# Optimization experiments

Hardware: AMD Instinct MI355X
Metric: run time of the kernel (lower is better)

## Reference

```python
import jax, jax.numpy as jnp
import numpy as np

MODES = 32
INPUT_MODES = 24
LAMBDA = 0.1
T_TOTAL = 1.0
EVAL_PTS = 200  # hardcoded in Circuit.forward


def _unitary_from_parameters(n, params):
    # Reconstruct a unitary from n**2-1 real SU(N)-generator coefficients:
    # Hermitian traceless H, then U = expm(iH) via eigh (differentiable).
    m = n * (n - 1) // 2
    re = params[:m]
    im = params[m:2 * m]
    d = params[2 * m:2 * m + n - 1]
    iu = jnp.triu_indices(n, 1)
    H = jnp.zeros((n, n), jnp.complex64).at[iu].set(re + 1j * im)
    H = H + H.conj().T
    diag = jnp.concatenate([d, -jnp.sum(d, keepdims=True)]).astype(jnp.complex64)
    H = H + jnp.diag(diag)
    w, V = jnp.linalg.eigh(H)  # H Hermitian
    return (V * jnp.exp(1j * w)[None, :]) @ V.conj().T


def setup_inputs() -> dict:
    key = jax.random.key(0)
    k1, k2, k3, k4, k5, k6 = jax.random.split(key, 6)
    B = 2048
    return {
        "A0_real": jax.random.normal(k1, (B, INPUT_MODES), jnp.float32),
        "A0_imag": jax.random.normal(k2, (B, INPUT_MODES), jnp.float32),
        "omega": jax.random.normal(k3, (MODES,), jnp.float32),
        "kappa": jax.random.uniform(k4, (MODES,), jnp.float32),
        "nonlinearity": jax.random.uniform(k5, (1,), jnp.float32),
        "params": (jax.random.uniform(k6, (MODES * MODES - 1,), jnp.float32) - 0.5) * (2.0 * np.pi),
    }


def reference(A0_real, A0_imag, omega, kappa, nonlinearity, params):
    c64 = jnp.complex64
    B = A0_real.shape[0]
    A0 = (A0_real + 1j * A0_imag).astype(c64)
    # pad: first input_modes from A0, rest ones (per forward)
    A_init = jnp.ones((B, MODES), c64).at[:, :INPUT_MODES].set(A0)

    U = _unitary_from_parameters(MODES, params)
    I = jnp.eye(MODES, dtype=c64)
    UtU = U.T @ U  # plain (non-conjugate) transpose, matching torch U.T
    mix = UtU @ jnp.linalg.inv(I * (1.0 + LAMBDA) - UtU)
    kappa2 = kappa.astype(c64) ** 2            # ode passes kappa**2
    sk = jnp.sqrt(kappa2)                      # diag_embed(kappa**0.5)
    T2 = -(sk[:, None] * (0.5 * I + mix)) * sk[None, :]  # constant in time
    nl2 = (nonlinearity[0].astype(c64)) ** 2   # ode passes nonlinearity**2
    om = omega.astype(c64)

    def f(A):  # time_evolution_operator, with diag matmuls fused elementwise
        freq = 1j * (om[None, :] + nl2 * (jnp.abs(A) ** 2))  # [B, modes]
        return freq * A + A @ T2.T  # correct_norm assumed identity passthrough

    dt = T_TOTAL / (EVAL_PTS - 1)

    def step(A, _):  # classic RK4 (fixed-step stand-in for dopri5)
        k1 = f(A)
        k2 = f(A + 0.5 * dt * k1)
        k3 = f(A + 0.5 * dt * k2)
        k4 = f(A + dt * k3)
        A = A + (dt / 6.0) * (k1 + 2.0 * k2 + 2.0 * k3 + k4)
        return A, A

    _, traj = jax.lax.scan(step, A_init, None, length=EVAL_PTS - 1)
    return jnp.concatenate([A_init[None], traj], axis=0)  # [200, B, modes] complex64
```

## Files before the change

kernel.cpp:

```cpp
#include <hip/hip_runtime.h>
#include <math.h>

#define NMODES 32
#define NPAIR 496
#define TAYLOR_N 12

__device__ float2 g_T2[NMODES * NMODES];

__device__ __forceinline__ float2 cmul(float2 a, float2 b) {
    return make_float2(a.x * b.x - a.y * b.y, a.x * b.y + a.y * b.x);
}

__global__ __launch_bounds__(1024) void setup_kernel(const float* __restrict__ params,
                                                     const float* __restrict__ kappa) {
    __shared__ float2 X[NMODES][NMODES];
    __shared__ float2 R[NMODES][NMODES];
    __shared__ float2 W[NMODES][NMODES];
    __shared__ float2 Aug[NMODES][2 * NMODES];
    __shared__ int sh_s;
    __shared__ float sh_scale;
    __shared__ int sh_piv;
    __shared__ float2 sh_pivrec;

    const int tid = threadIdx.x;
    const int i = tid >> 5;
    const int j = tid & 31;

    float2 h;
    if (i == j) {
        float d;
        if (i < 31) {
            d = params[2 * NPAIR + i];
        } else {
            d = 0.0f;
            for (int r = 0; r < 31; ++r) d -= params[2 * NPAIR + r];
        }
        h = make_float2(d, 0.0f);
    } else {
        int a = (i < j) ? i : j;
        int b = (i < j) ? j : i;
        int idx = 31 * a - (a * (a - 1)) / 2 + (b - a - 1);
        float re = params[idx];
        float im = params[NPAIR + idx];
        h = (i < j) ? make_float2(re, im) : make_float2(re, -im);
    }
    X[i][j] = h;
    __syncthreads();

    if (tid < 32) {
        float s = 0.0f;
        for (int c = 0; c < NMODES; ++c) {
            float2 v = X[tid][c];
            s += sqrtf(v.x * v.x + v.y * v.y);
        }
        for (int off = 16; off > 0; off >>= 1)
            s = fmaxf(s, __shfl_down(s, off));
        if (tid == 0) {
            int sc_n = 0;
            float sc = 1.0f;
            while (s > 0.25f && sc_n < 40) { s *= 0.5f; sc *= 0.5f; ++sc_n; }
            sh_s = sc_n;
            sh_scale = sc;
        }
    }
    __syncthreads();

    {
        float sc = sh_scale;
        float2 v = X[i][j];
        X[i][j] = make_float2(-v.y * sc, v.x * sc);
    }
    __syncthreads();

    R[i][j] = make_float2((i == j) ? 1.0f : 0.0f, 0.0f);
    __syncthreads();
    for (int k = TAYLOR_N; k >= 1; --k) {
        float2 acc = make_float2(0.0f, 0.0f);
        for (int kk = 0; kk < NMODES; ++kk) {
            float2 a = X[i][kk];
            float2 b = R[kk][j];
            acc.x = fmaf(a.x, b.x, fmaf(-a.y, b.y, acc.x));
            acc.y = fmaf(a.x, b.y, fmaf(a.y, b.x, acc.y));
        }
        __syncthreads();
        float invk = 1.0f / (float)k;
        R[i][j] = make_float2(((i == j) ? 1.0f : 0.0f) + acc.x * invk, acc.y * invk);
        __syncthreads();
    }

    {
        int s = sh_s;
        for (int q = 0; q < s; ++q) {
            float2 acc = make_float2(0.0f, 0.0f);
            for (int kk = 0; kk < NMODES; ++kk) {
                float2 a = R[i][kk];
                float2 b = R[kk][j];
                acc.x = fmaf(a.x, b.x, fmaf(-a.y, b.y, acc.x));
                acc.y = fmaf(a.x, b.y, fmaf(a.y, b.x, acc.y));
            }
            __syncthreads();
            R[i][j] = acc;
            __syncthreads();
        }
    }

    {
        float2 acc = make_float2(0.0f, 0.0f);
        for (int kk = 0; kk < NMODES; ++kk) {
            float2 a = R[kk][i];
            float2 b = R[kk][j];
            acc.x = fmaf(a.x, b.x, fmaf(-a.y, b.y, acc.x));
            acc.y = fmaf(a.x, b.y, fmaf(a.y, b.x, acc.y));
        }
        W[i][j] = acc;
    }
    __syncthreads();

    {
        float2 w = W[i][j];
        Aug[i][j] = make_float2(((i == j) ? 1.1f : 0.0f) - w.x, -w.y);
        Aug[i][j + NMODES] = w;
    }
    __syncthreads();

    for (int p = 0; p < NMODES; ++p) {
        if (tid < 32) {
            float2 v = Aug[tid][p];
            float mag = (tid >= p) ? (v.x * v.x + v.y * v.y) : -1.0f;
            int idx = tid;
            for (int off = 16; off > 0; off >>= 1) {
                float omg = __shfl_down(mag, off);
                int oi = __shfl_down(idx, off);
                if (omg > mag) { mag = omg; idx = oi; }
            }
            if (tid == 0) sh_piv = idx;
        }
        __syncthreads();
        int piv = sh_piv;
        if (piv != p && i == p) {
            float2 a0 = Aug[p][j], b0 = Aug[piv][j];
            float2 a1 = Aug[p][j + NMODES], b1 = Aug[piv][j + NMODES];
            Aug[p][j] = b0; Aug[piv][j] = a0;
            Aug[p][j + NMODES] = b1; Aug[piv][j + NMODES] = a1;
        }
        __syncthreads();
        if (tid == 0) {
            float2 d = Aug[p][p];
            float den = d.x * d.x + d.y * d.y;
            sh_pivrec = make_float2(d.x / den, -d.y / den);
        }
        __syncthreads();
        if (i == p) {
            float2 pr = sh_pivrec;
            Aug[p][j] = cmul(Aug[p][j], pr);
            Aug[p][j + NMODES] = cmul(Aug[p][j + NMODES], pr);
        }
        __syncthreads();
        float2 f = Aug[i][p];
        __syncthreads();
        if (i != p) {
            float2 rp0 = Aug[p][j];
            float2 rp1 = Aug[p][j + NMODES];
            float2 v0 = Aug[i][j];
            float2 v1 = Aug[i][j + NMODES];
            v0.x -= f.x * rp0.x - f.y * rp0.y;
            v0.y -= f.x * rp0.y + f.y * rp0.x;
            v1.x -= f.x * rp1.x - f.y * rp1.y;
            v1.y -= f.x * rp1.y + f.y * rp1.x;
            Aug[i][j] = v0;
            Aug[i][j + NMODES] = v1;
        }
        __syncthreads();
    }

    {
        float2 mix = Aug[i][j + NMODES];
        float kk2 = fabsf(kappa[i]) * fabsf(kappa[j]);
        float re = -kk2 * (((i == j) ? 0.5f : 0.0f) + mix.x);
        float im = -kk2 * mix.y;
        g_T2[i * NMODES + j] = make_float2(re, im);
    }
}

template<int CTRL>
__device__ __forceinline__ float2 dppshuf(float2 v) {
    return make_float2(
        __int_as_float(__builtin_amdgcn_mov_dpp(__float_as_int(v.x), CTRL, 0xF, 0xF, true)),
        __int_as_float(__builtin_amdgcn_mov_dpp(__float_as_int(v.y), CTRL, 0xF, 0xF, true)));
}

#define QP_X1 0xB1
#define QP_X2 0x4E
#define QP_X3 0x1B
#define HM_X7 0x141
#define RM_XF 0x140

__device__ __forceinline__ void cfma(float2& acc, float2 c, float2 w) {
    acc.x = fmaf(c.x, w.x, fmaf(-c.y, w.y, acc.x));
    acc.y = fmaf(c.x, w.y, fmaf(c.y, w.x, acc.y));
}

__device__ __forceinline__ float bperm(int idx, float v) {
    return __int_as_float(__builtin_amdgcn_ds_bpermute(idx, __float_as_int(v)));
}

__device__ __forceinline__ float2 feval(const float2* __restrict__ t2,
                                        float2 z, float om, float nl2,
                                        int bp0, int bp1) {
    float2 w1 = dppshuf<QP_X1>(z);
    float2 w2 = dppshuf<QP_X2>(z);
    float2 w3 = dppshuf<QP_X3>(z);
    float2 w7 = dppshuf<HM_X7>(z);
    float2 wF = dppshuf<RM_XF>(z);
    float2 w4 = dppshuf<QP_X3>(w7);
    float2 w5 = dppshuf<QP_X2>(w7);
    float2 w6 = dppshuf<QP_X1>(w7);
    float2 w8 = dppshuf<HM_X7>(wF);
    float2 wC = dppshuf<QP_X3>(wF);
    float2 wD = dppshuf<QP_X2>(wF);
    float2 wE = dppshuf<QP_X1>(wF);
    float2 w9 = dppshuf<QP_X1>(w8);
    float2 wA = dppshuf<QP_X2>(w8);
    float2 wB = dppshuf<QP_X3>(w8);

    float2 a0 = make_float2(0.0f, 0.0f), a1 = make_float2(0.0f, 0.0f);
    float2 a2 = make_float2(0.0f, 0.0f), a3 = make_float2(0.0f, 0.0f);
    cfma(a0, t2[0],  z);
    cfma(a1, t2[1],  w1);
    cfma(a2, t2[2],  w2);
    cfma(a3, t2[3],  w3);
    cfma(a0, t2[4],  w4);
    cfma(a1, t2[5],  w5);
    cfma(a2, t2[6],  w6);
    cfma(a3, t2[7],  w7);
    cfma(a0, t2[8],  w8);
    cfma(a1, t2[9],  w9);
    cfma(a2, t2[10], wA);
    cfma(a3, t2[11], wB);
    cfma(a0, t2[12], wC);
    cfma(a1, t2[13], wD);
    cfma(a2, t2[14], wE);
    cfma(a3, t2[15], wF);

    float px = (a0.x + a1.x) + (a2.x + a3.x);
    float py = (a0.y + a1.y) + (a2.y + a3.y);
    float kx = bperm(bp0, px) + bperm(bp1, px);
    float ky = bperm(bp0, py) + bperm(bp1, py);

    float wf = fmaf(nl2, fmaf(z.x, z.x, z.y * z.y), om);
    return make_float2(kx - wf * z.y, ky + wf * z.x);
}

__global__ __launch_bounds__(64) void ode_kernel(const float* __restrict__ A0r,
                                                 const float* __restrict__ A0i,
                                                 const float* __restrict__ omega,
                                                 const float* __restrict__ nln,
                                                 float* __restrict__ out,
                                                 long long out_size) {
    const int lane = threadIdx.x;
    const int r = lane >> 4;
    const int p = lane & 15;
    const int ho = r & 1;
    const int hr = (r == 1 || r == 2) ? 1 : 0;
    const int mstar = 16 * hr + p;
    const int bp0 = 4 * mstar;
    const int bp1 = bp0 + 128;
    const int b = blockIdx.x;

    float2 t2[16];
    {
        const int row_g = 16 * ho + p;
#pragma unroll
        for (int s = 0; s < 16; ++s)
            t2[s] = g_T2[row_g * 32 + 16 * hr + (p ^ s)];
    }

    const float om = omega[mstar];
    const float nl = nln[0];
    const float nl2 = nl * nl;
    const float dt = 1.0f / 199.0f;
    const float hdt = 0.5f * dt;
    const float sdt = dt / 6.0f;

    __shared__ float2 ainit[32];
    if (lane < 32) {
        float2 v;
        if (lane < 24) v = make_float2(A0r[b * 24 + lane], A0i[b * 24 + lane]);
        else           v = make_float2(1.0f, 0.0f);
        ainit[lane] = v;
    }
    __syncthreads();
    float2 a = ainit[mstar];

    long long o = (long long)b * 32 + lane;
    if (lane < 32 && o < out_size) out[o] = a.x;

    for (int t = 1; t < 200; ++t) {
        float2 k1 = feval(t2, a, om, nl2, bp0, bp1);
        float2 z = make_float2(fmaf(hdt, k1.x, a.x), fmaf(hdt, k1.y, a.y));
        float2 k2 = feval(t2, z, om, nl2, bp0, bp1);
        z = make_float2(fmaf(hdt, k2.x, a.x), fmaf(hdt, k2.y, a.y));
        float2 k3 = feval(t2, z, om, nl2, bp0, bp1);
        z = make_float2(fmaf(dt, k3.x, a.x), fmaf(dt, k3.y, a.y));
        float2 k4 = feval(t2, z, om, nl2, bp0, bp1);

        a.x = fmaf(sdt, fmaf(2.0f, k2.x + k3.x, k1.x + k4.x), a.x);
        a.y = fmaf(sdt, fmaf(2.0f, k2.y + k3.y, k1.y + k4.y), a.y);

        o += 65536;
        if (lane < 32 && o < out_size) out[o] = a.x;
    }
}

extern "C" void kernel_launch(void* const* d_in, const int* in_sizes, int n_in,
                              void* d_out, int out_size, void* d_ws, size_t ws_size,
                              hipStream_t stream) {
    const float* A0r = (const float*)d_in[0];
    const float* A0i = (const float*)d_in[1];
    const float* omega = (const float*)d_in[2];
    const float* kappa = (const float*)d_in[3];
    const float* nln = (const float*)d_in[4];
    const float* params = (const float*)d_in[5];

    setup_kernel<<<1, 1024, 0, stream>>>(params, kappa);
    ode_kernel<<<2048, 64, 0, stream>>>(A0r, A0i, omega, nln,
                                        (float*)d_out, (long long)out_size);
}
```

Baseline: 395.3 us.

## Replace bpermute reductions with permlane32/16 swaps and remap lanes per mode

Remaps the 64 lanes so each half-wave owns all 32 modes, with the two halves holding complementary column halves of T2. The cross-half reduction now uses permlane32_swap instead of two ds_bpermute ops. The shuffle seed comes from a permlane16_swap (or ds_swizzle fallback) so the DPP butterfly covers the right column block. The aim is to take LDS-routed permutes off the serial RK4 dependency chain, at the cost of one extra cross-lane op per stage and reliance on gfx950-specific builtins.

```diff
diff --git a/kernel.cpp b/kernel.cpp
--- a/kernel.cpp
+++ b/kernel.cpp
@@ -195,6 +195,8 @@
 #define HM_X7 0x141
 #define RM_XF 0x140
 
+typedef unsigned int v2u __attribute__((ext_vector_type(2)));
+
 __device__ __forceinline__ void cfma(float2& acc, float2 c, float2 w) {
     acc.x = fmaf(c.x, w.x, fmaf(-c.y, w.y, acc.x));
     acc.y = fmaf(c.x, w.y, fmaf(c.y, w.x, acc.y));
@@ -204,14 +206,47 @@
     return __int_as_float(__builtin_amdgcn_ds_bpermute(idx, __float_as_int(v)));
 }
 
+__device__ __forceinline__ float comb32(float x, int bp0) {
+#if __has_builtin(__builtin_amdgcn_permlane32_swap)
+    v2u r = __builtin_amdgcn_permlane32_swap(__float_as_uint(x), __float_as_uint(x),
+                                             false, false);
+    return __uint_as_float(r.x) + __uint_as_float(r.y);
+#else
+    return bperm(bp0, x) + bperm(bp0 + 128, x);
+#endif
+}
+
+template<int MASK>
+__device__ __forceinline__ float2 swzshuf(float2 v) {
+    return make_float2(
+        __int_as_float(__builtin_amdgcn_ds_swizzle(__float_as_int(v.x), MASK)),
+        __int_as_float(__builtin_amdgcn_ds_swizzle(__float_as_int(v.y), MASK)));
+}
+
+__device__ __forceinline__ float2 seed_of(float2 y, bool upper) {
+#if __has_builtin(__builtin_amdgcn_permlane16_swap)
+    v2u rx = __builtin_amdgcn_permlane16_swap(__float_as_uint(y.x), __float_as_uint(y.x),
+                                              false, false);
+    v2u ry = __builtin_amdgcn_permlane16_swap(__float_as_uint(y.y), __float_as_uint(y.y),
+                                              false, false);
+    return make_float2(upper ? __uint_as_float(rx.y) : __uint_as_float(rx.x),
+                       upper ? __uint_as_float(ry.y) : __uint_as_float(ry.x));
+#else
+    float2 sw = swzshuf<0x401F>(y);
+    int rrow = (int)(threadIdx.x >> 4);
+    bool mid = (rrow == 1) || (rrow == 2);
+    return make_float2(mid ? sw.x : y.x, mid ? sw.y : y.y);
+#endif
+}
+
 __device__ __forceinline__ float2 feval(const float2* __restrict__ t2,
-                                        float2 z, float om, float nl2,
-                                        int bp0, int bp1) {
-    float2 w1 = dppshuf<QP_X1>(z);
-    float2 w2 = dppshuf<QP_X2>(z);
-    float2 w3 = dppshuf<QP_X3>(z);
-    float2 w7 = dppshuf<HM_X7>(z);
-    float2 wF = dppshuf<RM_XF>(z);
+                                        float2 seed, float2 zloc,
+                                        float om, float nl2, int bp0) {
+    float2 w1 = dppshuf<QP_X1>(seed);
+    float2 w2 = dppshuf<QP_X2>(seed);
+    float2 w3 = dppshuf<QP_X3>(seed);
+    float2 w7 = dppshuf<HM_X7>(seed);
+    float2 wF = dppshuf<RM_XF>(seed);
     float2 w4 = dppshuf<QP_X3>(w7);
     float2 w5 = dppshuf<QP_X2>(w7);
     float2 w6 = dppshuf<QP_X1>(w7);
@@ -225,7 +260,7 @@
 
     float2 a0 = make_float2(0.0f, 0.0f), a1 = make_float2(0.0f, 0.0f);
     float2 a2 = make_float2(0.0f, 0.0f), a3 = make_float2(0.0f, 0.0f);
-    cfma(a0, t2[0],  z);
+    cfma(a0, t2[0],  seed);
     cfma(a1, t2[1],  w1);
     cfma(a2, t2[2],  w2);
     cfma(a3, t2[3],  w3);
@@ -244,11 +279,11 @@
 
     float px = (a0.x + a1.x) + (a2.x + a3.x);
     float py = (a0.y + a1.y) + (a2.y + a3.y);
-    float kx = bperm(bp0, px) + bperm(bp1, px);
-    float ky = bperm(bp0, py) + bperm(bp1, py);
-
-    float wf = fmaf(nl2, fmaf(z.x, z.x, z.y * z.y), om);
-    return make_float2(kx - wf * z.y, ky + wf * z.x);
+    float kx = comb32(px, bp0);
+    float ky = comb32(py, bp0);
+
+    float wf = fmaf(nl2, fmaf(zloc.x, zloc.x, zloc.y * zloc.y), om);
+    return make_float2(kx - wf * zloc.y, ky + wf * zloc.x);
 }
 
 __global__ __launch_bounds__(64) void ode_kernel(const float* __restrict__ A0r,
@@ -258,22 +293,17 @@
                                                  float* __restrict__ out,
                                                  long long out_size) {
     const int lane = threadIdx.x;
-    const int r = lane >> 4;
     const int p = lane & 15;
-    const int ho = r & 1;
-    const int hr = (r == 1 || r == 2) ? 1 : 0;
-    const int mstar = 16 * hr + p;
+    const int mstar = lane & 31;
+    const bool upper = lane >= 32;
+    const int hs = upper ? 1 : 0;
     const int bp0 = 4 * mstar;
-    const int bp1 = bp0 + 128;
     const int b = blockIdx.x;
 
     float2 t2[16];
-    {
-        const int row_g = 16 * ho + p;
 #pragma unroll
-        for (int s = 0; s < 16; ++s)
-            t2[s] = g_T2[row_g * 32 + 16 * hr + (p ^ s)];
-    }
+    for (int s = 0; s < 16; ++s)
+        t2[s] = g_T2[mstar * 32 + 16 * hs + (p ^ s)];
 
     const float om = omega[mstar];
     const float nl = nln[0];
@@ -295,17 +325,23 @@
     long long o = (long long)b * 32 + lane;
     if (lane < 32 && o < out_size) out[o] = a.x;
 
+    float2 s0 = seed_of(a, upper);
+
     for (int t = 1; t < 200; ++t) {
-        float2 k1 = feval(t2, a, om, nl2, bp0, bp1);
-        float2 z = make_float2(fmaf(hdt, k1.x, a.x), fmaf(hdt, k1.y, a.y));
-        float2 k2 = feval(t2, z, om, nl2, bp0, bp1);
-        z = make_float2(fmaf(hdt, k2.x, a.x), fmaf(hdt, k2.y, a.y));
-        float2 k3 = feval(t2, z, om, nl2, bp0, bp1);
-        z = make_float2(fmaf(dt, k3.x, a.x), fmaf(dt, k3.y, a.y));
-        float2 k4 = feval(t2, z, om, nl2, bp0, bp1);
+        float2 k1 = feval(t2, s0, a, om, nl2, bp0);
+        float2 y = make_float2(fmaf(hdt, k1.x, a.x), fmaf(hdt, k1.y, a.y));
+        float2 sd = seed_of(y, upper);
+        float2 k2 = feval(t2, sd, y, om, nl2, bp0);
+        y = make_float2(fmaf(hdt, k2.x, a.x), fmaf(hdt, k2.y, a.y));
+        sd = seed_of(y, upper);
+        float2 k3 = feval(t2, sd, y, om, nl2, bp0);
+        y = make_float2(fmaf(dt, k3.x, a.x), fmaf(dt, k3.y, a.y));
+        sd = seed_of(y, upper);
+        float2 k4 = feval(t2, sd, y, om, nl2, bp0);
 
         a.x = fmaf(sdt, fmaf(2.0f, k2.x + k3.x, k1.x + k4.x), a.x);
         a.y = fmaf(sdt, fmaf(2.0f, k2.y + k3.y, k1.y + k4.y), a.y);
+        s0 = seed_of(a, upper);
 
         o += 65536;
         if (lane < 32 && o < out_size) out[o] = a.x;
```

Result: slower. 418.6 us (+5.9%).

## Split blocks between DPP-shuffle and LDS-broadcast ODE paths to balance units

Applied to the files above, without the earlier changes.

Even-indexed blocks keep the DPP/bpermute cross-lane matvec. Odd-indexed blocks use a new path in which each lane pair computes one mode's row dot product from an LDS-broadcast state vector, with __syncthreads between RK4 stages. The aim is to spread work across the DPP/VALU and LDS pipes when waves of both kinds share a CU. It adds code size and divergent register pressure, and the LDS path puts four block barriers in every step.

```diff
diff --git a/kernel.cpp b/kernel.cpp
--- a/kernel.cpp
+++ b/kernel.cpp
@@ -182,6 +182,7 @@
     }
 }
 
+
 template<int CTRL>
 __device__ __forceinline__ float2 dppshuf(float2 v) {
     return make_float2(
@@ -204,9 +205,9 @@
     return __int_as_float(__builtin_amdgcn_ds_bpermute(idx, __float_as_int(v)));
 }
 
-__device__ __forceinline__ float2 feval(const float2* __restrict__ t2,
-                                        float2 z, float om, float nl2,
-                                        int bp0, int bp1) {
+__device__ __forceinline__ float2 feval_dpp(const float2* __restrict__ t2,
+                                            float2 z, float om, float nl2,
+                                            int bp0, int bp1) {
     float2 w1 = dppshuf<QP_X1>(z);
     float2 w2 = dppshuf<QP_X2>(z);
     float2 w3 = dppshuf<QP_X3>(z);
@@ -251,6 +252,158 @@
     return make_float2(kx - wf * z.y, ky + wf * z.x);
 }
 
+__device__ void ode_dpp(int b, int lane,
+                        const float* __restrict__ A0r,
+                        const float* __restrict__ A0i,
+                        const float* __restrict__ omega,
+                        const float* __restrict__ nln,
+                        float* __restrict__ out, long long out_size) {
+    const int r = lane >> 4;
+    const int p = lane & 15;
+    const int ho = r & 1;
+    const int hr = (r == 1 || r == 2) ? 1 : 0;
+    const int mstar = 16 * hr + p;
+    const int bp0 = 4 * mstar;
+    const int bp1 = bp0 + 128;
+
+    float2 t2[16];
+    {
+        const int row_g = 16 * ho + p;
+#pragma unroll
+        for (int s = 0; s < 16; ++s)
+            t2[s] = g_T2[row_g * 32 + 16 * hr + (p ^ s)];
+    }
+
+    const float om = omega[mstar];
+    const float nl = nln[0];
+    const float nl2 = nl * nl;
+    const float dt = 1.0f / 199.0f;
+    const float hdt = 0.5f * dt;
+    const float sdt = dt / 6.0f;
+
+    __shared__ float2 ainit[32];
+    if (lane < 32) {
+        float2 v;
+        if (lane < 24) v = make_float2(A0r[b * 24 + lane], A0i[b * 24 + lane]);
+        else           v = make_float2(1.0f, 0.0f);
+        ainit[lane] = v;
+    }
+    __syncthreads();
+    float2 a = ainit[mstar];
+
+    long long o = (long long)b * 32 + lane;
+    if (lane < 32 && o < out_size) out[o] = a.x;
+
+    for (int t = 1; t < 200; ++t) {
+        float2 k1 = feval_dpp(t2, a, om, nl2, bp0, bp1);
+        float2 z = make_float2(fmaf(hdt, k1.x, a.x), fmaf(hdt, k1.y, a.y));
+        float2 k2 = feval_dpp(t2, z, om, nl2, bp0, bp1);
+        z = make_float2(fmaf(hdt, k2.x, a.x), fmaf(hdt, k2.y, a.y));
+        float2 k3 = feval_dpp(t2, z, om, nl2, bp0, bp1);
+        z = make_float2(fmaf(dt, k3.x, a.x), fmaf(dt, k3.y, a.y));
+        float2 k4 = feval_dpp(t2, z, om, nl2, bp0, bp1);
+
+        a.x = fmaf(sdt, fmaf(2.0f, k2.x + k3.x, k1.x + k4.x), a.x);
+        a.y = fmaf(sdt, fmaf(2.0f, k2.y + k3.y, k1.y + k4.y), a.y);
+
+        o += 65536;
+        if (lane < 32 && o < out_size) out[o] = a.x;
+    }
+}
+
+__device__ __forceinline__ float2 f_eval_lds(const float4* __restrict__ xq,
+                                             float2 ym,
+                                             const float2* __restrict__ t2h,
+                                             float om, float nl2) {
+    float2 acc0 = make_float2(0.0f, 0.0f);
+    float2 acc1 = make_float2(0.0f, 0.0f);
+#pragma unroll
+    for (int j = 0; j < 8; ++j) {
+        float4 v = xq[j];
+        float2 ta = t2h[2 * j];
+        float2 tb = t2h[2 * j + 1];
+        acc0.x = fmaf(ta.x, v.x, acc0.x);
+        acc0.x = fmaf(-ta.y, v.y, acc0.x);
+        acc0.y = fmaf(ta.x, v.y, acc0.y);
+        acc0.y = fmaf(ta.y, v.x, acc0.y);
+        acc1.x = fmaf(tb.x, v.z, acc1.x);
+        acc1.x = fmaf(-tb.y, v.w, acc1.x);
+        acc1.y = fmaf(tb.x, v.w, acc1.y);
+        acc1.y = fmaf(tb.y, v.z, acc1.y);
+    }
+    float2 acc = make_float2(acc0.x + acc1.x, acc0.y + acc1.y);
+    acc.x += __shfl_xor(acc.x, 1);
+    acc.y += __shfl_xor(acc.y, 1);
+    float w = fmaf(nl2, fmaf(ym.x, ym.x, ym.y * ym.y), om);
+    return make_float2(acc.x - w * ym.y, acc.y + w * ym.x);
+}
+
+__device__ void ode_lds(int b, int lane,
+                        const float* __restrict__ A0r,
+                        const float* __restrict__ A0i,
+                        const float* __restrict__ omega,
+                        const float* __restrict__ nln,
+                        float* __restrict__ out, long long out_size) {
+    const int m = lane >> 1;
+    const int h = lane & 1;
+
+    float2 t2h[16];
+#pragma unroll
+    for (int j = 0; j < 16; ++j) t2h[j] = g_T2[m * NMODES + h * 16 + j];
+
+    const float om = omega[m];
+    const float nl = nln[0];
+    const float nl2 = nl * nl;
+    const float dt = 1.0f / 199.0f;
+    const float hdt = 0.5f * dt;
+    const float sdt = dt / 6.0f;
+
+    float2 a;
+    if (m < 24) a = make_float2(A0r[b * 24 + m], A0i[b * 24 + m]);
+    else        a = make_float2(1.0f, 0.0f);
+
+    __shared__ __align__(16) float2 xbuf[36];
+    const int swi = m + ((m >= 16) ? 2 : 0);
+    const float4* xq = reinterpret_cast<const float4*>(xbuf) + 9 * h;
+
+    if (h == 0) {
+        long long o0 = (long long)b * 32 + m;
+        if (o0 < out_size) out[o0] = a.x;
+        xbuf[swi] = a;
+    }
+    __syncthreads();
+
+    long long o = (long long)b * 32 + m;
+    for (int t = 1; t < 200; ++t) {
+        float2 k1 = f_eval_lds(xq, a, t2h, om, nl2);
+        float2 y2 = make_float2(fmaf(hdt, k1.x, a.x), fmaf(hdt, k1.y, a.y));
+        if (h == 0) xbuf[swi] = y2;
+        __syncthreads();
+
+        float2 k2 = f_eval_lds(xq, y2, t2h, om, nl2);
+        float2 y3 = make_float2(fmaf(hdt, k2.x, a.x), fmaf(hdt, k2.y, a.y));
+        if (h == 0) xbuf[swi] = y3;
+        __syncthreads();
+
+        float2 k3 = f_eval_lds(xq, y3, t2h, om, nl2);
+        float2 y4 = make_float2(fmaf(dt, k3.x, a.x), fmaf(dt, k3.y, a.y));
+        if (h == 0) xbuf[swi] = y4;
+        __syncthreads();
+
+        float2 k4 = f_eval_lds(xq, y4, t2h, om, nl2);
+
+        a.x = fmaf(sdt, k1.x + 2.0f * k2.x + 2.0f * k3.x + k4.x, a.x);
+        a.y = fmaf(sdt, k1.y + 2.0f * k2.y + 2.0f * k3.y + k4.y, a.y);
+
+        o += 65536;
+        if (h == 0) {
+            xbuf[swi] = a;
+            if (o < out_size) out[o] = a.x;
+        }
+        __syncthreads();
+    }
+}
+
 __global__ __launch_bounds__(64) void ode_kernel(const float* __restrict__ A0r,
                                                  const float* __restrict__ A0i,
                                                  const float* __restrict__ omega,
@@ -258,57 +411,11 @@
                                                  float* __restrict__ out,
                                                  long long out_size) {
     const int lane = threadIdx.x;
-    const int r = lane >> 4;
-    const int p = lane & 15;
-    const int ho = r & 1;
-    const int hr = (r == 1 || r == 2) ? 1 : 0;
-    const int mstar = 16 * hr + p;
-    const int bp0 = 4 * mstar;
-    const int bp1 = bp0 + 128;
     const int b = blockIdx.x;
-
-    float2 t2[16];
-    {
-        const int row_g = 16 * ho + p;
-#pragma unroll
-        for (int s = 0; s < 16; ++s)
-            t2[s] = g_T2[row_g * 32 + 16 * hr + (p ^ s)];
-    }
-
-    const float om = omega[mstar];
-    const float nl = nln[0];
-    const float nl2 = nl * nl;
-    const float dt = 1.0f / 199.0f;
-    const float hdt = 0.5f * dt;
-    const float sdt = dt / 6.0f;
-
-    __shared__ float2 ainit[32];
-    if (lane < 32) {
-        float2 v;
-        if (lane < 24) v = make_float2(A0r[b * 24 + lane], A0i[b * 24 + lane]);
-        else           v = make_float2(1.0f, 0.0f);
-        ainit[lane] = v;
-    }
-    __syncthreads();
-    float2 a = ainit[mstar];
-
-    long long o = (long long)b * 32 + lane;
-    if (lane < 32 && o < out_size) out[o] = a.x;
-
-    for (int t = 1; t < 200; ++t) {
-        float2 k1 = feval(t2, a, om, nl2, bp0, bp1);
-        float2 z = make_float2(fmaf(hdt, k1.x, a.x), fmaf(hdt, k1.y, a.y));
-        float2 k2 = feval(t2, z, om, nl2, bp0, bp1);
-        z = make_float2(fmaf(hdt, k2.x, a.x), fmaf(hdt, k2.y, a.y));
-        float2 k3 = feval(t2, z, om, nl2, bp0, bp1);
-        z = make_float2(fmaf(dt, k3.x, a.x), fmaf(dt, k3.y, a.y));
-        float2 k4 = feval(t2, z, om, nl2, bp0, bp1);
-
-        a.x = fmaf(sdt, fmaf(2.0f, k2.x + k3.x, k1.x + k4.x), a.x);
-        a.y = fmaf(sdt, fmaf(2.0f, k2.y + k3.y, k1.y + k4.y), a.y);
-
-        o += 65536;
-        if (lane < 32 && o < out_size) out[o] = a.x;
+    if ((b & 1) == 0) {
+        ode_dpp(b, lane, A0r, A0i, omega, nln, out, out_size);
+    } else {
+        ode_lds(b, lane, A0r, A0i, omega, nln, out, out_size);
     }
 }
 
```

After: 393.8 us. No clear change (-0.4%).
